# Kernel optimization log

Measured on AMD Instinct MI355X. Metric: run time of the kernel, lower is better.

The kernel has to match this reference:

```python
import jax, jax.numpy as jnp
import numpy as np

DIM = 512
HEADS = 16
DHEAD = DIM // HEADS
SQRT_DIM = float(np.sqrt(DIM))


def sinusoidal_pe(length, dim):
    # Transformer-XL style sinusoidal positional embedding, shape (length, dim)
    pos = jnp.arange(length, dtype=jnp.float32)[:, None]
    i = jnp.arange(0, dim, 2, dtype=jnp.float32)
    div = jnp.exp(-(jnp.log(jnp.float32(10000.0)) * i / dim))[None, :]
    ang = pos * div
    pe = jnp.zeros((length, dim), dtype=jnp.float32)
    pe = pe.at[:, 0::2].set(jnp.sin(ang)).at[:, 1::2].set(jnp.cos(ang))
    return pe


def rel_shift(x):
    # x: (B, H, L, M) -> Transformer-XL relative shift
    B, H, L, M = x.shape
    x = jnp.concatenate([jnp.zeros((B, H, L, 1), x.dtype), x], axis=-1)  # (B,H,L,M+1)
    x = x.reshape(B, H, M + 1, L)[:, :, 1:, :].reshape(B, H, L, M)
    return x


def setup_inputs() -> dict:
    key = jax.random.key(0)
    ks = jax.random.split(key, 16)
    B, L = 8, 1024
    s = 0.02
    return {
        "query": jax.random.normal(ks[0], (B, L, DIM), jnp.float32),
        "key_in": jax.random.normal(ks[1], (B, L, DIM), jnp.float32),
        "value": jax.random.normal(ks[2], (B, L, DIM), jnp.float32),
        "Wq": jax.random.normal(ks[3], (DIM, DIM), jnp.float32) * s,
        "bq": jnp.zeros((DIM,), jnp.float32),
        "Wk": jax.random.normal(ks[4], (DIM, DIM), jnp.float32) * s,
        "bk": jnp.zeros((DIM,), jnp.float32),
        "Wv": jax.random.normal(ks[5], (DIM, DIM), jnp.float32) * s,
        "bv": jnp.zeros((DIM,), jnp.float32),
        "Wpos": jax.random.normal(ks[6], (DIM, DIM), jnp.float32) * s,
        "u_bias": jax.random.normal(ks[7], (HEADS, DHEAD), jnp.float32) * s,
        "v_bias": jax.random.normal(ks[8], (HEADS, DHEAD), jnp.float32) * s,
        "Wo": jax.random.normal(ks[9], (DIM, DIM), jnp.float32) * s,
        "bo": jnp.zeros((DIM,), jnp.float32),
    }


def reference(query, key_in, value, Wq, bq, Wk, bk, Wv, bv, Wpos, u_bias, v_bias, Wo, bo):
    B, L, _ = value.shape
    pe = sinusoidal_pe(L, DIM)                                   # (L, dim)
    q = (query @ Wq.T + bq).reshape(B, L, HEADS, DHEAD)          # (B,L,H,d)
    k = (key_in @ Wk.T + bk).reshape(B, L, HEADS, DHEAD)         # (B,L,H,d)
    v = (value @ Wv.T + bv).reshape(B, L, HEADS, DHEAD)          # (B,L,H,d)
    pos = (pe @ Wpos.T).reshape(L, HEADS, DHEAD)                 # (L,H,d)

    content_score = jnp.einsum("blhd,bmhd->bhlm", q + u_bias, k)
    pos_score = jnp.einsum("blhd,mhd->bhlm", q + v_bias, pos)
    pos_score = rel_shift(pos_score)
    score = (content_score + pos_score) / SQRT_DIM               # (B,H,L,L)
    attn = jax.nn.softmax(score, axis=-1)
    context = jnp.einsum("bhlm,bmhd->blhd", attn, v).reshape(B, L, DIM)
    return context @ Wo.T + bo
```

## Files before the change

kernel.cpp:

```cpp
#include <hip/hip_runtime.h>
#include <hip/hip_bf16.h>
#include <cstddef>

typedef _Float16 f16;
typedef _Float16 f16x8 __attribute__((ext_vector_type(8)));
typedef _Float16 f16x4 __attribute__((ext_vector_type(4)));
typedef _Float16 f16x2 __attribute__((ext_vector_type(2)));
typedef float    f32x4 __attribute__((ext_vector_type(4)));

#define MFMA16(a,b,c)   __builtin_amdgcn_mfma_f32_16x16x32_f16((a),(b),(c),0,0,0)
#define MFMA16K16(a,b,c) __builtin_amdgcn_mfma_f32_16x16x16f16((a),(b),(c),0,0,0)

#if __has_builtin(__builtin_amdgcn_exp2f)
#define EXP2(x) __builtin_amdgcn_exp2f(x)
#else
#define EXP2(x) __expf((x) * 0.6931471805599453f)
#endif

__device__ __forceinline__ void gload16(const void* g, void* lds) {
  __builtin_amdgcn_global_load_lds((const __attribute__((address_space(1))) void*)g,
                                   (__attribute__((address_space(3))) void*)lds, 16, 0, 0);
}

__global__ __launch_bounds__(256) void conv_w(
    const float* __restrict__ w0, const float* __restrict__ w1,
    const float* __restrict__ w2, const float* __restrict__ w3,
    const float* __restrict__ w4, f16* __restrict__ dst)
{
  const int idx = blockIdx.x * 256 + threadIdx.x;
  const int seg = idx >> 16;
  const int r   = idx & 65535;
  const float* s = seg == 0 ? w0 : seg == 1 ? w1 : seg == 2 ? w2 : seg == 3 ? w3 : w4;
  float4 v = ((const float4*)s)[r];
  f16x4 h = { (f16)v.x, (f16)v.y, (f16)v.z, (f16)v.w };
  ((f16x4*)(dst + ((size_t)seg << 18)))[r] = h;
}

__global__ __launch_bounds__(256) void pe16_kernel(f16* __restrict__ pe) {
  const int l = blockIdx.x;
  const int p = threadIdx.x;
  const float divv = expf(-(logf(10000.0f) * (2.0f * (float)p)) / 512.0f);
  const float ang  = (float)l * divv;
  f16x2 o = { (f16)sinf(ang), (f16)cosf(ang) };
  *(f16x2*)(pe + (size_t)l * 512 + 2 * p) = o;
}

template<int MODE, bool AF16>
__global__ __launch_bounds__(256) void gemm_k512(
    const void* __restrict__ Ap, const f16* __restrict__ Wf,
    const float* __restrict__ bias, void* __restrict__ Cp)
{
  __shared__ __align__(16) char Asm[8192];
  __shared__ __align__(16) char Bsm[8192];

  const int tid   = threadIdx.x;
  const int gm0   = blockIdx.x * 64;
  const int gn0   = blockIdx.y * 64;
  const int lane  = tid & 63, w = tid >> 6;
  const int row16 = lane & 15, grp = lane >> 4;
  const int wm = w & 1, wn = w >> 1;
  const int lr8  = lane >> 3;
  const int swcb = ((lane & 7) ^ lr8) * 16;

  f32x4 acc[2][2];
  for (int i = 0; i < 2; ++i) for (int j = 0; j < 2; ++j)
    for (int r = 0; r < 4; ++r) acc[i][j][r] = 0.f;

  for (int k0 = 0; k0 < 512; k0 += 64) {
    __syncthreads();
#pragma unroll
    for (int i = 0; i < 2; ++i) {
      const int rB = w * 8 + i * 32;
      gload16((const char*)Wf + ((size_t)(gn0 + rB + lr8)) * 1024 + (size_t)k0 * 2 + swcb,
              Bsm + rB * 128);
    }
    if constexpr (AF16) {
#pragma unroll
      for (int i = 0; i < 2; ++i) {
        const int rA = w * 8 + i * 32;
        gload16((const char*)Ap + ((size_t)(gm0 + rA + lr8)) * 1024 + (size_t)k0 * 2 + swcb,
                Asm + rA * 128);
      }
    } else {
#pragma unroll
      for (int i = 0; i < 4; ++i) {
        const int u = tid + i * 256;
        const int row = u >> 4, cf = (u & 15) * 4;
        float4 av = *(const float4*)((const float*)Ap + (size_t)(gm0 + row) * 512 + k0 + cf);
        f16x4 hv = { (f16)av.x, (f16)av.y, (f16)av.z, (f16)av.w };
        *(f16x4*)(Asm + row * 128 + ((cf * 2) ^ ((row & 7) * 16))) = hv;
      }
    }
    asm volatile("s_waitcnt vmcnt(0)" ::: "memory");
    __syncthreads();
#pragma unroll
    for (int kk = 0; kk < 64; kk += 32) {
      const int cb = (kk + 8 * grp) * 2;
      const int ra0 = wm * 32 + row16,      ra1 = ra0 + 16;
      const int rb0 = wn * 32 + row16,      rb1 = rb0 + 16;
      f16x8 a0 = *(const f16x8*)(Asm + ra0 * 128 + (cb ^ ((ra0 & 7) * 16)));
      f16x8 a1 = *(const f16x8*)(Asm + ra1 * 128 + (cb ^ ((ra1 & 7) * 16)));
      f16x8 b0 = *(const f16x8*)(Bsm + rb0 * 128 + (cb ^ ((rb0 & 7) * 16)));
      f16x8 b1 = *(const f16x8*)(Bsm + rb1 * 128 + (cb ^ ((rb1 & 7) * 16)));
      acc[0][0] = MFMA16(a0, b0, acc[0][0]);
      acc[0][1] = MFMA16(a0, b1, acc[0][1]);
      acc[1][0] = MFMA16(a1, b0, acc[1][0]);
      acc[1][1] = MFMA16(a1, b1, acc[1][1]);
    }
  }

  for (int fi = 0; fi < 2; ++fi) {
    for (int fj = 0; fj < 2; ++fj) {
      const int gc = gn0 + wn * 32 + fj * 16 + row16;
      float bval;
      if constexpr (MODE == 2) bval = 0.f; else bval = bias[gc];
      for (int r = 0; r < 4; ++r) {
        const int gr = gm0 + wm * 32 + fi * 16 + grp * 4 + r;
        const float v = acc[fi][fj][r] + bval;
        if constexpr (MODE == 0) {
          const int b = gr >> 10, l = gr & 1023, h = gc >> 5, d = gc & 31;
          ((f16*)Cp)[(((size_t)(b * 16 + h)) * 1024 + l) * 32 + d] = (f16)v;
        } else if constexpr (MODE == 1) {
          const int b = gr >> 10, l = gr & 1023, h = gc >> 5, d = gc & 31;
          ((f16*)Cp)[(((size_t)(b * 16 + h)) * 32 + d) * 1024 + l] = (f16)v;
        } else if constexpr (MODE == 2) {
          const int h = gc >> 5, d = gc & 31;
          ((f16*)Cp)[(((size_t)h) * 1024 + gr) * 32 + d] = (f16)v;
        } else {
          ((float*)Cp)[(size_t)gr * 512 + gc] = v;
        }
      }
    }
  }
}

__global__ __launch_bounds__(256) void attn_kernel(
    const f16* __restrict__ Qf, const f16* __restrict__ Kf,
    const f16* __restrict__ Vt, const f16* __restrict__ Pos,
    const float* __restrict__ ubias, const float* __restrict__ vbias,
    f16* __restrict__ ctx)
{
  __shared__ f16 P_lds[17][1028];

  const int tid   = threadIdx.x;
  const int w     = tid >> 6, lane = tid & 63;
  const int row16 = lane & 15, grp = lane >> 4;
  const int b = blockIdx.z, h = blockIdx.y;
  const int l0 = blockIdx.x * 16;

  const size_t bh = (size_t)(b * 16 + h);
  const f16* Qb = Qf + bh * 1024 * 32;
  const f16* Kb = Kf + bh * 1024 * 32;
  const f16* Vb = Vt + bh * 32 * 1024;
  const f16* Pb = Pos + (size_t)h * 1024 * 32;

  const f32x4 z4 = {0.f, 0.f, 0.f, 0.f};
  const float kpre = 0.0637587157f;

  f16x8 qu, qv, qv2;
  {
    f16x8 qraw = *(const f16x8*)(Qb + (size_t)(l0 + row16) * 32 + 8 * grp);
    const int r2 = l0 + 16 + row16;
    f16x8 q2 = *(const f16x8*)(Qb + (size_t)(r2 < 1024 ? r2 : 1023) * 32 + 8 * grp);
#pragma unroll
    for (int e = 0; e < 8; ++e) {
      const float u = ubias[h * 32 + 8 * grp + e];
      const float v = vbias[h * 32 + 8 * grp + e];
      qu[e]  = (f16)((float)qraw[e] + u);
      qv[e]  = (f16)((float)qraw[e] + v);
      qv2[e] = (f16)((float)q2[e]   + v);
    }
  }

  if (tid < 17) {
    f16x4 z = {(f16)0.f, (f16)0.f, (f16)0.f, (f16)0.f};
    *(f16x4*)&P_lds[tid][1024] = z;
  }

#pragma unroll 4
  for (int c = 0; c < 16; ++c) {
    const int jc = w * 16 + c;
    f16x8 pf = *(const f16x8*)(Pb + (size_t)(jc * 16 + row16) * 32 + 8 * grp);
    f32x4 p0 = MFMA16(pf, qv,  z4);
    f32x4 p1 = MFMA16(pf, qv2, z4);
    const int j0 = jc * 16 + grp * 4;
    {
      f16x4 vv = { (f16)(p0[0] * kpre), (f16)(p0[1] * kpre),
                   (f16)(p0[2] * kpre), (f16)(p0[3] * kpre) };
      *(f16x4*)&P_lds[row16][j0] = vv;
    }
    if (row16 == 0) {
      f16x4 vv = { (f16)(p1[0] * kpre), (f16)(p1[1] * kpre),
                   (f16)(p1[2] * kpre), (f16)(p1[3] * kpre) };
      *(f16x4*)&P_lds[16][j0] = vv;
    }
  }
  __syncthreads();

  float psum = 0.f;
  f32x4 od[2];
#pragma unroll
  for (int hh = 0; hh < 2; ++hh) for (int r = 0; r < 4; ++r) od[hh][r] = 0.f;

  const int  c1   = 1023 - l0 - row16;
  const f16* Prow = &P_lds[row16][0];
  const f16* Vr0  = Vb + (size_t)row16 * 1024;
  const f16* Vr1  = Vb + (size_t)(16 + row16) * 1024;

  for (int ti = 0; ti < 4; ++ti) {
    const int mbase = w * 256 + ti * 64;

    f32x4 st[4];
#pragma unroll
    for (int c = 0; c < 4; ++c) {
      f16x8 kf = *(const f16x8*)(Kb + (size_t)(mbase + c * 16 + row16) * 32 + 8 * grp);
      st[c] = MFMA16(kf, qu, z4);
    }

    float sh[4][4];
    const bool unifB = (mbase >= l0 + 17);
    const bool unifA = (mbase + 62 <= l0);
    if (unifB | unifA) {
      const f16* pp = Prow + mbase + grp * 4 + c1 + (unifB ? 3 : 0);
#pragma unroll
      for (int c = 0; c < 4; ++c)
#pragma unroll
        for (int r = 0; r < 4; ++r) sh[c][r] = (float)pp[c * 16 + r];
    } else {
#pragma unroll
      for (int c = 0; c < 4; ++c)
#pragma unroll
        for (int r = 0; r < 4; ++r) {
          const int jA = mbase + c * 16 + grp * 4 + r + c1;
          sh[c][r] = (float)Prow[jA + (jA >= 1025 ? 3 : 0)];
        }
    }

#pragma unroll
    for (int c = 0; c < 4; ++c) {
      float p[4];
#pragma unroll
      for (int r = 0; r < 4; ++r) {
        p[r] = EXP2(fmaf(st[c][r], kpre, sh[c][r]));
        psum += p[r];
      }
      f16x4 pa = { (f16)p[0], (f16)p[1], (f16)p[2], (f16)p[3] };
      const int m0 = mbase + c * 16 + grp * 4;
      f16x4 v0 = *(const f16x4*)(Vr0 + m0);
      f16x4 v1 = *(const f16x4*)(Vr1 + m0);
      od[0] = MFMA16K16(pa, v0, od[0]);
      od[1] = MFMA16K16(pa, v1, od[1]);
    }
  }

  float l1 = psum + __shfl_xor(psum, 16);
  l1 += __shfl_xor(l1, 32);

  __syncthreads();
  float* mo = (float*)&P_lds[0][0];
  float* ls = mo + 4 * 16 * 32;
#pragma unroll
  for (int hh = 0; hh < 2; ++hh)
#pragma unroll
    for (int r = 0; r < 4; ++r)
      mo[(w * 16 + grp * 4 + r) * 32 + hh * 16 + row16] = od[hh][r];
  if (grp == 0) ls[w * 16 + row16] = l1;
  __syncthreads();

  const int q = tid >> 4, dp = tid & 15;
  const float Ls = ls[q] + ls[16 + q] + ls[32 + q] + ls[48 + q];
  float o0 = 0.f, o1 = 0.f;
#pragma unroll
  for (int ww = 0; ww < 4; ++ww) {
    o0 += mo[(ww * 16 + q) * 32 + 2 * dp];
    o1 += mo[(ww * 16 + q) * 32 + 2 * dp + 1];
  }
  const float inv = 1.f / Ls;
  const size_t oidx = ((size_t)(b * 1024 + l0 + q)) * 512 + h * 32 + 2 * dp;
  f16x2 o2 = { (f16)(o0 * inv), (f16)(o1 * inv) };
  *(f16x2*)(ctx + oidx) = o2;
}

extern "C" void kernel_launch(void* const* d_in, const int* in_sizes, int n_in,
                              void* d_out, int out_size, void* d_ws, size_t ws_size,
                              hipStream_t stream) {
  const float* query  = (const float*)d_in[0];
  const float* key_in = (const float*)d_in[1];
  const float* value  = (const float*)d_in[2];
  const float* Wq = (const float*)d_in[3];
  const float* bq = (const float*)d_in[4];
  const float* Wk = (const float*)d_in[5];
  const float* bk = (const float*)d_in[6];
  const float* Wv = (const float*)d_in[7];
  const float* bv = (const float*)d_in[8];
  const float* Wpos = (const float*)d_in[9];
  const float* ub   = (const float*)d_in[10];
  const float* vb   = (const float*)d_in[11];
  const float* Wo = (const float*)d_in[12];
  const float* bo = (const float*)d_in[13];
  float* out = (float*)d_out;

  char* ws = (char*)d_ws;
  f16* W16  = (f16*)(ws);
  f16* pe16 = (f16*)(ws + 2621440);
  f16* Qf   = (f16*)(ws + 3670016);
  f16* Kf   = (f16*)(ws + 12058624);
  f16* Vtf  = (f16*)(ws + 20447232);
  f16* Pf   = (f16*)(ws + 28835840);
  f16* ctx  = (f16*)(ws + 29884416);

  conv_w<<<1280, 256, 0, stream>>>(Wq, Wk, Wv, Wpos, Wo, W16);
  pe16_kernel<<<1024, 256, 0, stream>>>(pe16);
  gemm_k512<0, false><<<dim3(128, 8), 256, 0, stream>>>(query,  W16,          bq, Qf);
  gemm_k512<0, false><<<dim3(128, 8), 256, 0, stream>>>(key_in, W16 + 262144, bk, Kf);
  gemm_k512<1, false><<<dim3(128, 8), 256, 0, stream>>>(value,  W16 + 524288, bv, Vtf);
  gemm_k512<2, true ><<<dim3(16,  8), 256, 0, stream>>>(pe16,   W16 + 786432, nullptr, Pf);
  attn_kernel<<<dim3(64, 16, 8), 256, 0, stream>>>(Qf, Kf, Vtf, Pf, ub, vb, ctx);
  gemm_k512<3, true ><<<dim3(128, 8), 256, 0, stream>>>(ctx, W16 + 1048576, bo, out);
}
```

Measured before the change: 345.7 us.

## Double-buffer GEMMs, fuse QKV projections into one launch, use K32 MFMA for PV

The projection GEMMs now double-buffer their LDS tiles, prefetching the next K-slice (register-staged fp32 A, async B) while the current one is consumed. The three Q/K/V projections are merged into one launch over a z-dimension. In attention, probabilities are staged through a per-wave LDS tile so P·V uses the 16x16x32 MFMA with 8-wide V loads. Row sums now come from an MFMA against a ones vector instead of scalar adds and shuffles. This trades more LDS and extra LDS round-trips for fewer launches and better load/compute overlap.

```diff
diff --git a/kernel.cpp b/kernel.cpp
--- a/kernel.cpp
+++ b/kernel.cpp
@@ -8,8 +8,7 @@
 typedef _Float16 f16x2 __attribute__((ext_vector_type(2)));
 typedef float    f32x4 __attribute__((ext_vector_type(4)));
 
-#define MFMA16(a,b,c)   __builtin_amdgcn_mfma_f32_16x16x32_f16((a),(b),(c),0,0,0)
-#define MFMA16K16(a,b,c) __builtin_amdgcn_mfma_f32_16x16x16f16((a),(b),(c),0,0,0)
+#define MFMA16(a,b,c) __builtin_amdgcn_mfma_f32_16x16x32_f16((a),(b),(c),0,0,0)
 
 #if __has_builtin(__builtin_amdgcn_exp2f)
 #define EXP2(x) __builtin_amdgcn_exp2f(x)
@@ -45,13 +44,21 @@
   *(f16x2*)(pe + (size_t)l * 512 + 2 * p) = o;
 }
 
-template<int MODE, bool AF16>
-__global__ __launch_bounds__(256) void gemm_k512(
-    const void* __restrict__ Ap, const f16* __restrict__ Wf,
-    const float* __restrict__ bias, void* __restrict__ Cp)
+__global__ __launch_bounds__(256) void gemm_qkv(
+    const float* __restrict__ q_in, const float* __restrict__ k_in,
+    const float* __restrict__ v_in, const f16* __restrict__ W16,
+    const float* __restrict__ bq, const float* __restrict__ bk,
+    const float* __restrict__ bv,
+    f16* __restrict__ Qf, f16* __restrict__ Kf, f16* __restrict__ Vtf)
 {
-  __shared__ __align__(16) char Asm[8192];
-  __shared__ __align__(16) char Bsm[8192];
+  __shared__ __align__(16) char Asm[2][8192];
+  __shared__ __align__(16) char Bsm[2][8192];
+
+  const int z = blockIdx.z;
+  const float* Ap   = z == 0 ? q_in : z == 1 ? k_in : v_in;
+  const f16*   Wf   = W16 + (size_t)z * 262144;
+  const float* bias = z == 0 ? bq : z == 1 ? bk : bv;
+  f16*         Cp   = z == 0 ? Qf : z == 1 ? Kf : Vtf;
 
   const int tid   = threadIdx.x;
   const int gm0   = blockIdx.x * 64;
@@ -63,67 +70,157 @@
   const int swcb = ((lane & 7) ^ lr8) * 16;
 
   f32x4 acc[2][2];
-  for (int i = 0; i < 2; ++i) for (int j = 0; j < 2; ++j)
-    for (int r = 0; r < 4; ++r) acc[i][j][r] = 0.f;
-
-  for (int k0 = 0; k0 < 512; k0 += 64) {
-    __syncthreads();
-#pragma unroll
-    for (int i = 0; i < 2; ++i) {
-      const int rB = w * 8 + i * 32;
-      gload16((const char*)Wf + ((size_t)(gn0 + rB + lr8)) * 1024 + (size_t)k0 * 2 + swcb,
-              Bsm + rB * 128);
-    }
-    if constexpr (AF16) {
-#pragma unroll
-      for (int i = 0; i < 2; ++i) {
-        const int rA = w * 8 + i * 32;
-        gload16((const char*)Ap + ((size_t)(gm0 + rA + lr8)) * 1024 + (size_t)k0 * 2 + swcb,
-                Asm + rA * 128);
-      }
-    } else {
-#pragma unroll
-      for (int i = 0; i < 4; ++i) {
-        const int u = tid + i * 256;
-        const int row = u >> 4, cf = (u & 15) * 4;
-        float4 av = *(const float4*)((const float*)Ap + (size_t)(gm0 + row) * 512 + k0 + cf);
-        f16x4 hv = { (f16)av.x, (f16)av.y, (f16)av.z, (f16)av.w };
-        *(f16x4*)(Asm + row * 128 + ((cf * 2) ^ ((row & 7) * 16))) = hv;
-      }
-    }
-    asm volatile("s_waitcnt vmcnt(0)" ::: "memory");
-    __syncthreads();
+#pragma unroll
+  for (int i = 0; i < 2; ++i)
+#pragma unroll
+    for (int j = 0; j < 2; ++j)
+#pragma unroll
+      for (int r = 0; r < 4; ++r) acc[i][j][r] = 0.f;
+
+  float4 areg[4];
+#define QKV_ALOAD(k0) do {                                                   \
+_Pragma("unroll")                                                            \
+  for (int i = 0; i < 4; ++i) {                                              \
+    const int u = tid + i * 256; const int row = u >> 4, cf = (u & 15) * 4;  \
+    areg[i] = *(const float4*)(Ap + (size_t)(gm0 + row) * 512 + (k0) + cf);  \
+  } } while (0)
+#define QKV_AWRITE(buf) do {                                                 \
+_Pragma("unroll")                                                            \
+  for (int i = 0; i < 4; ++i) {                                              \
+    const int u = tid + i * 256; const int row = u >> 4, cf = (u & 15) * 4;  \
+    f16x4 hv = { (f16)areg[i].x, (f16)areg[i].y, (f16)areg[i].z, (f16)areg[i].w }; \
+    *(f16x4*)(Asm[buf] + row * 128 + ((cf * 2) ^ ((row & 7) * 16))) = hv;    \
+  } } while (0)
+#define QKV_BSTAGE(buf, k0) do {                                             \
+_Pragma("unroll")                                                            \
+  for (int i = 0; i < 2; ++i) {                                              \
+    const int rB = w * 8 + i * 32;                                           \
+    gload16((const char*)Wf + ((size_t)(gn0 + rB + lr8)) * 1024 +            \
+            (size_t)(k0) * 2 + swcb, Bsm[buf] + rB * 128);                   \
+  } } while (0)
+
+  QKV_ALOAD(0);
+  QKV_BSTAGE(0, 0);
+  QKV_AWRITE(0);
+  asm volatile("s_waitcnt vmcnt(0)" ::: "memory");
+  __syncthreads();
+
+  int cur = 0;
+  for (int t = 0; t < 8; ++t) {
+    if (t < 7) { QKV_ALOAD((t + 1) * 64); QKV_BSTAGE(cur ^ 1, (t + 1) * 64); }
 #pragma unroll
     for (int kk = 0; kk < 64; kk += 32) {
       const int cb = (kk + 8 * grp) * 2;
-      const int ra0 = wm * 32 + row16,      ra1 = ra0 + 16;
-      const int rb0 = wn * 32 + row16,      rb1 = rb0 + 16;
-      f16x8 a0 = *(const f16x8*)(Asm + ra0 * 128 + (cb ^ ((ra0 & 7) * 16)));
-      f16x8 a1 = *(const f16x8*)(Asm + ra1 * 128 + (cb ^ ((ra1 & 7) * 16)));
-      f16x8 b0 = *(const f16x8*)(Bsm + rb0 * 128 + (cb ^ ((rb0 & 7) * 16)));
-      f16x8 b1 = *(const f16x8*)(Bsm + rb1 * 128 + (cb ^ ((rb1 & 7) * 16)));
+      const int ra0 = wm * 32 + row16, ra1 = ra0 + 16;
+      const int rb0 = wn * 32 + row16, rb1 = rb0 + 16;
+      f16x8 a0 = *(const f16x8*)(Asm[cur] + ra0 * 128 + (cb ^ ((ra0 & 7) * 16)));
+      f16x8 a1 = *(const f16x8*)(Asm[cur] + ra1 * 128 + (cb ^ ((ra1 & 7) * 16)));
+      f16x8 b0 = *(const f16x8*)(Bsm[cur] + rb0 * 128 + (cb ^ ((rb0 & 7) * 16)));
+      f16x8 b1 = *(const f16x8*)(Bsm[cur] + rb1 * 128 + (cb ^ ((rb1 & 7) * 16)));
       acc[0][0] = MFMA16(a0, b0, acc[0][0]);
       acc[0][1] = MFMA16(a0, b1, acc[0][1]);
       acc[1][0] = MFMA16(a1, b0, acc[1][0]);
       acc[1][1] = MFMA16(a1, b1, acc[1][1]);
     }
-  }
-
-  for (int fi = 0; fi < 2; ++fi) {
+    if (t < 7) QKV_AWRITE(cur ^ 1);
+    asm volatile("s_waitcnt vmcnt(0)" ::: "memory");
+    __syncthreads();
+    cur ^= 1;
+  }
+
+#pragma unroll
+  for (int fi = 0; fi < 2; ++fi)
+#pragma unroll
+    for (int fj = 0; fj < 2; ++fj) {
+      const int gc = gn0 + wn * 32 + fj * 16 + row16;
+      const float bval = bias[gc];
+#pragma unroll
+      for (int r = 0; r < 4; ++r) {
+        const int gr = gm0 + wm * 32 + fi * 16 + grp * 4 + r;
+        const float v = acc[fi][fj][r] + bval;
+        const int b = gr >> 10, l = gr & 1023, h = gc >> 5, d = gc & 31;
+        if (z != 2) {
+          Cp[(((size_t)(b * 16 + h)) * 1024 + l) * 32 + d] = (f16)v;
+        } else {
+          Cp[(((size_t)(b * 16 + h)) * 32 + d) * 1024 + l] = (f16)v;
+        }
+      }
+    }
+}
+
+template<int MODE>
+__global__ __launch_bounds__(256) void gemm_f16(
+    const f16* __restrict__ Ap, const f16* __restrict__ Wf,
+    const float* __restrict__ bias, void* __restrict__ Cp)
+{
+  __shared__ __align__(16) char Asm[2][8192];
+  __shared__ __align__(16) char Bsm[2][8192];
+
+  const int tid   = threadIdx.x;
+  const int gm0   = blockIdx.x * 64;
+  const int gn0   = blockIdx.y * 64;
+  const int lane  = tid & 63, w = tid >> 6;
+  const int row16 = lane & 15, grp = lane >> 4;
+  const int wm = w & 1, wn = w >> 1;
+  const int lr8  = lane >> 3;
+  const int swcb = ((lane & 7) ^ lr8) * 16;
+
+  f32x4 acc[2][2];
+#pragma unroll
+  for (int i = 0; i < 2; ++i)
+#pragma unroll
+    for (int j = 0; j < 2; ++j)
+#pragma unroll
+      for (int r = 0; r < 4; ++r) acc[i][j][r] = 0.f;
+
+#define F16_STAGE(buf, k0) do {                                              \
+_Pragma("unroll")                                                            \
+  for (int i = 0; i < 2; ++i) {                                              \
+    const int rr = w * 8 + i * 32;                                           \
+    gload16((const char*)Ap + ((size_t)(gm0 + rr + lr8)) * 1024 +            \
+            (size_t)(k0) * 2 + swcb, Asm[buf] + rr * 128);                   \
+    gload16((const char*)Wf + ((size_t)(gn0 + rr + lr8)) * 1024 +            \
+            (size_t)(k0) * 2 + swcb, Bsm[buf] + rr * 128);                   \
+  } } while (0)
+
+  F16_STAGE(0, 0);
+  asm volatile("s_waitcnt vmcnt(0)" ::: "memory");
+  __syncthreads();
+
+  int cur = 0;
+  for (int t = 0; t < 8; ++t) {
+    if (t < 7) F16_STAGE(cur ^ 1, (t + 1) * 64);
+#pragma unroll
+    for (int kk = 0; kk < 64; kk += 32) {
+      const int cb = (kk + 8 * grp) * 2;
+      const int ra0 = wm * 32 + row16, ra1 = ra0 + 16;
+      const int rb0 = wn * 32 + row16, rb1 = rb0 + 16;
+      f16x8 a0 = *(const f16x8*)(Asm[cur] + ra0 * 128 + (cb ^ ((ra0 & 7) * 16)));
+      f16x8 a1 = *(const f16x8*)(Asm[cur] + ra1 * 128 + (cb ^ ((ra1 & 7) * 16)));
+      f16x8 b0 = *(const f16x8*)(Bsm[cur] + rb0 * 128 + (cb ^ ((rb0 & 7) * 16)));
+      f16x8 b1 = *(const f16x8*)(Bsm[cur] + rb1 * 128 + (cb ^ ((rb1 & 7) * 16)));
+      acc[0][0] = MFMA16(a0, b0, acc[0][0]);
+      acc[0][1] = MFMA16(a0, b1, acc[0][1]);
+      acc[1][0] = MFMA16(a1, b0, acc[1][0]);
+      acc[1][1] = MFMA16(a1, b1, acc[1][1]);
+    }
+    asm volatile("s_waitcnt vmcnt(0)" ::: "memory");
+    __syncthreads();
+    cur ^= 1;
+  }
+
+#pragma unroll
+  for (int fi = 0; fi < 2; ++fi)
+#pragma unroll
     for (int fj = 0; fj < 2; ++fj) {
       const int gc = gn0 + wn * 32 + fj * 16 + row16;
       float bval;
       if constexpr (MODE == 2) bval = 0.f; else bval = bias[gc];
+#pragma unroll
       for (int r = 0; r < 4; ++r) {
         const int gr = gm0 + wm * 32 + fi * 16 + grp * 4 + r;
         const float v = acc[fi][fj][r] + bval;
-        if constexpr (MODE == 0) {
-          const int b = gr >> 10, l = gr & 1023, h = gc >> 5, d = gc & 31;
-          ((f16*)Cp)[(((size_t)(b * 16 + h)) * 1024 + l) * 32 + d] = (f16)v;
-        } else if constexpr (MODE == 1) {
-          const int b = gr >> 10, l = gr & 1023, h = gc >> 5, d = gc & 31;
-          ((f16*)Cp)[(((size_t)(b * 16 + h)) * 32 + d) * 1024 + l] = (f16)v;
-        } else if constexpr (MODE == 2) {
+        if constexpr (MODE == 2) {
           const int h = gc >> 5, d = gc & 31;
           ((f16*)Cp)[(((size_t)h) * 1024 + gr) * 32 + d] = (f16)v;
         } else {
@@ -131,7 +228,6 @@
         }
       }
     }
-  }
 }
 
 __global__ __launch_bounds__(256) void attn_kernel(
@@ -141,6 +237,7 @@
     f16* __restrict__ ctx)
 {
   __shared__ f16 P_lds[17][1028];
+  __shared__ f16 ptile[4][16][72];
 
   const int tid   = threadIdx.x;
   const int w     = tid >> 6, lane = tid & 63;
@@ -197,15 +294,20 @@
   }
   __syncthreads();
 
-  float psum = 0.f;
-  f32x4 od[2];
-#pragma unroll
-  for (int hh = 0; hh < 2; ++hh) for (int r = 0; r < 4; ++r) od[hh][r] = 0.f;
+  f32x4 od[2], od2;
+#pragma unroll
+  for (int hh = 0; hh < 2; ++hh)
+#pragma unroll
+    for (int r = 0; r < 4; ++r) od[hh][r] = 0.f;
+#pragma unroll
+  for (int r = 0; r < 4; ++r) od2[r] = 0.f;
+
+  f16x8 ones;
+#pragma unroll
+  for (int e = 0; e < 8; ++e) ones[e] = (f16)1.f;
 
   const int  c1   = 1023 - l0 - row16;
   const f16* Prow = &P_lds[row16][0];
-  const f16* Vr0  = Vb + (size_t)row16 * 1024;
-  const f16* Vr1  = Vb + (size_t)(16 + row16) * 1024;
 
   for (int ti = 0; ti < 4; ++ti) {
     const int mbase = w * 256 + ti * 64;
@@ -240,21 +342,23 @@
     for (int c = 0; c < 4; ++c) {
       float p[4];
 #pragma unroll
-      for (int r = 0; r < 4; ++r) {
+      for (int r = 0; r < 4; ++r)
         p[r] = EXP2(fmaf(st[c][r], kpre, sh[c][r]));
-        psum += p[r];
+      f16x4 pv = { (f16)p[0], (f16)p[1], (f16)p[2], (f16)p[3] };
+      *(f16x4*)&ptile[w][row16][c * 16 + grp * 4] = pv;
+    }
+
+#pragma unroll
+    for (int kc = 0; kc < 2; ++kc) {
+      f16x8 pa = *(const f16x8*)&ptile[w][row16][kc * 32 + 8 * grp];
+      od2 = MFMA16(pa, ones, od2);
+#pragma unroll
+      for (int hh = 0; hh < 2; ++hh) {
+        f16x8 vf = *(const f16x8*)(Vb + (size_t)(hh * 16 + row16) * 1024 + mbase + kc * 32 + 8 * grp);
+        od[hh] = MFMA16(pa, vf, od[hh]);
       }
-      f16x4 pa = { (f16)p[0], (f16)p[1], (f16)p[2], (f16)p[3] };
-      const int m0 = mbase + c * 16 + grp * 4;
-      f16x4 v0 = *(const f16x4*)(Vr0 + m0);
-      f16x4 v1 = *(const f16x4*)(Vr1 + m0);
-      od[0] = MFMA16K16(pa, v0, od[0]);
-      od[1] = MFMA16K16(pa, v1, od[1]);
-    }
-  }
-
-  float l1 = psum + __shfl_xor(psum, 16);
-  l1 += __shfl_xor(l1, 32);
+    }
+  }
 
   __syncthreads();
   float* mo = (float*)&P_lds[0][0];
@@ -264,7 +368,10 @@
 #pragma unroll
     for (int r = 0; r < 4; ++r)
       mo[(w * 16 + grp * 4 + r) * 32 + hh * 16 + row16] = od[hh][r];
-  if (grp == 0) ls[w * 16 + row16] = l1;
+  if (row16 == 0) {
+#pragma unroll
+    for (int r = 0; r < 4; ++r) ls[w * 16 + grp * 4 + r] = od2[r];
+  }
   __syncthreads();
 
   const int q = tid >> 4, dp = tid & 15;
@@ -311,10 +418,9 @@
 
   conv_w<<<1280, 256, 0, stream>>>(Wq, Wk, Wv, Wpos, Wo, W16);
   pe16_kernel<<<1024, 256, 0, stream>>>(pe16);
-  gemm_k512<0, false><<<dim3(128, 8), 256, 0, stream>>>(query,  W16,          bq, Qf);
-  gemm_k512<0, false><<<dim3(128, 8), 256, 0, stream>>>(key_in, W16 + 262144, bk, Kf);
-  gemm_k512<1, false><<<dim3(128, 8), 256, 0, stream>>>(value,  W16 + 524288, bv, Vtf);
-  gemm_k512<2, true ><<<dim3(16,  8), 256, 0, stream>>>(pe16,   W16 + 786432, nullptr, Pf);
+  gemm_qkv<<<dim3(128, 8, 3), 256, 0, stream>>>(query, key_in, value, W16,
+                                                bq, bk, bv, Qf, Kf, Vtf);
+  gemm_f16<2><<<dim3(16,  8), 256, 0, stream>>>(pe16, W16 + 786432, nullptr, Pf);
   attn_kernel<<<dim3(64, 16, 8), 256, 0, stream>>>(Qf, Kf, Vtf, Pf, ub, vb, ctx);
-  gemm_k512<3, true ><<<dim3(128, 8), 256, 0, stream>>>(ctx, W16 + 1048576, bo, out);
-}
+  gemm_f16<3><<<dim3(128, 8), 256, 0, stream>>>(ctx, W16 + 1048576, bo, out);
+}
```

After: 317.8 us. 1.09x faster.
